# Kernel tuning notes

Measured on AMD Instinct MI355X. Metric: run time of the kernel, lower is better.

Reference implementation:

```python
import jax, jax.numpy as jnp
import numpy as np

NEG = -10000.0
EPS = 1e-5

B, N, H, DEPTH = 4096, 64, 128, 3
H2 = H // 2


def setup_inputs() -> dict:
    key = jax.random.key(0)
    k1, k2, k3 = jax.random.split(key, 3)
    hidden_states = jax.random.normal(k1, (B, N, H), dtype=jnp.float32)
    li_vector_num = jax.random.randint(k2, (B,), 0, N + 1, dtype=jnp.int32)
    Ws = jax.random.normal(k3, (DEPTH, H, H2), dtype=jnp.float32) * (1.0 / np.sqrt(H))
    bs = jnp.zeros((DEPTH, H2), dtype=jnp.float32)
    ln_w = jnp.ones((DEPTH, H2), dtype=jnp.float32)
    ln_b = jnp.zeros((DEPTH, H2), dtype=jnp.float32)
    return {"hidden_states": hidden_states, "li_vector_num": li_vector_num,
            "Ws": Ws, "bs": bs, "ln_w": ln_w, "ln_b": ln_b}


def _subgraph(hidden_states, Ws, bs, ln_w, ln_b, li_vector_num):
    b, n, h = hidden_states.shape
    # padding mask: -10000 for invalid vectors (i >= li_vector_num), per polyline
    pad = jnp.where(jnp.arange(n)[None, :] >= li_vector_num[:, None], NEG, 0.0)
    pad = pad.astype(hidden_states.dtype)[:, :, None]  # [B,N,1]
    hs = hidden_states
    for l in range(Ws.shape[0]):
        # MLP: linear -> layernorm -> relu
        x = jnp.einsum('bnh,hk->bnk', hs, Ws[l]) + bs[l]
        mu = jnp.mean(x, axis=-1, keepdims=True)
        var = jnp.mean((x - mu) ** 2, axis=-1, keepdims=True)
        x = ln_w[l] * (x - mu) * jax.lax.rsqrt(var + EPS) + ln_b[l]
        enc = jax.nn.relu(x)  # [B,N,H2]
        m = enc + pad  # masked encoded states
        # leave-one-out max over vector dim via top-2 trick (replaces O(N^2) loop)
        top2 = jax.lax.top_k(jnp.swapaxes(m, 1, 2), 2)[0]  # [B,H2,2]
        top1b = top2[..., 0][:, None, :]  # [B,1,H2]
        top2b = top2[..., 1][:, None, :]  # [B,1,H2]
        loo = jnp.where(m == top1b, top2b, top1b)  # max over i != j
        loo = jnp.maximum(loo, m + NEG)            # faithful: j itself at -10000
        loo = jnp.maximum(loo, 0.0)                # torch.max(max_hidden, zeros)
        hs = jnp.concatenate([enc, loo], axis=-1)  # [B,N,H]
    return jnp.max(hs, axis=1)  # [B,H]


def reference(hidden_states, li_vector_num, Ws, bs, ln_w, ln_b):
    return _subgraph(hidden_states, Ws, bs, ln_w, ln_b, li_vector_num)
```

## Files before the change

kernel.cpp:

```cpp
#include <hip/hip_runtime.h>
#include <hip/hip_bf16.h>

#define NEGV (-10000.0f)
#define EPSV (1e-5f)
#define NINF (-3.4e38f)

typedef __attribute__((ext_vector_type(8))) short short8;
typedef __attribute__((ext_vector_type(4))) float floatx4;

constexpr int Bsz = 4096, Nv = 64, Hd = 128, DEPTH = 3, H2 = 64;
constexpr int HSTR = 136;

struct alignas(8) BH4 { __hip_bfloat162 a, b; };

__device__ __forceinline__ unsigned short f2b(float f) {
    unsigned int u = __builtin_bit_cast(unsigned int, f);
    u += 0x7fffu + ((u >> 16) & 1u);
    return (unsigned short)(u >> 16);
}

__device__ __forceinline__ void t2ins(float& t1, float& t2, float v) {
    float lo = fminf(t1, v); t1 = fmaxf(t1, v); t2 = fmaxf(t2, lo);
}
__device__ __forceinline__ void t2merge(float& t1, float& t2, float o1, float o2) {
    float lo = fminf(t1, o1); t1 = fmaxf(t1, o1); t2 = fmaxf(fmaxf(t2, o2), lo);
}

__global__ void prep_w(const float* __restrict__ Ws, unsigned short* __restrict__ wt) {
    int idx = blockIdx.x * 256 + threadIdx.x;
    if (idx < DEPTH * 8192) {
        int l = idx >> 13, o = idx & 8191;
        int j = o & 7, q = (o >> 3) & 63, hi = (o >> 9) & 3, kt = o >> 11;
        int k = kt * 32 + hi * 8 + j;
        int srccol = (q & 15) * 4 + (q >> 4);
        wt[idx] = f2b(Ws[l * 8192 + k * 64 + srccol]);
    }
}

__global__ __launch_bounds__(256, 2)
void subgraph_kernel(const float* __restrict__ hidden, const int* __restrict__ lvn,
                     const unsigned short* __restrict__ wt,
                     const float* __restrict__ bsv, const float* __restrict__ lnw,
                     const float* __restrict__ lnb, float* __restrict__ out)
{
    __shared__ __hip_bfloat16 hsw[4][Nv][HSTR];

    const int t = threadIdx.x;
    const int lane = t & 63, wid = t >> 6;
    const int b = blockIdx.x * 4 + wid;
    const int lr = lane & 15, hi = lane >> 4;
    const int L = lvn[b];

    __hip_bfloat16 (*hs)[HSTR] = hsw[wid];

    float madd[4][4];
#pragma unroll
    for (int rt = 0; rt < 4; ++rt)
#pragma unroll
        for (int reg = 0; reg < 4; ++reg)
            madd[rt][reg] = ((rt * 16 + hi * 4 + reg) >= L) ? NEGV : 0.0f;

    const float4* ab = (const float4*)(hidden + (size_t)b * Nv * Hd);
    float encmax[4], loomax[4];

#pragma unroll
    for (int l = 0; l < DEPTH; ++l) {
        const short8* wfrag = (const short8*)(wt + l * 8192);

        floatx4 acc[4][4];
#pragma unroll
        for (int rt = 0; rt < 4; ++rt)
#pragma unroll
            for (int ct = 0; ct < 4; ++ct) { floatx4 z = {0.f,0.f,0.f,0.f}; acc[rt][ct] = z; }

#pragma unroll
        for (int kt = 0; kt < 4; ++kt) {
            short8 af[4];
            if (l == 0) {
#pragma unroll
                for (int rt = 0; rt < 4; ++rt) {
                    int fi = (rt * 16 + lr) * 32 + kt * 8 + hi * 2;
                    float4 f0 = ab[fi], f1 = ab[fi + 1];
                    union { short8 s; __hip_bfloat162 h[4]; } u;
                    u.h[0] = __float22bfloat162_rn(make_float2(f0.x, f0.y));
                    u.h[1] = __float22bfloat162_rn(make_float2(f0.z, f0.w));
                    u.h[2] = __float22bfloat162_rn(make_float2(f1.x, f1.y));
                    u.h[3] = __float22bfloat162_rn(make_float2(f1.z, f1.w));
                    af[rt] = u.s;
                }
            } else {
#pragma unroll
                for (int rt = 0; rt < 4; ++rt)
                    af[rt] = *(const short8*)&hs[rt * 16 + lr][kt * 32 + hi * 8];
            }
#pragma unroll
            for (int ct = 0; ct < 4; ++ct) {
                short8 bf = wfrag[(kt * 4 + hi) * 64 + ct * 16 + lr];
#pragma unroll
                for (int rt = 0; rt < 4; ++rt)
                    acc[rt][ct] = __builtin_amdgcn_mfma_f32_16x16x32_bf16(af[rt], bf, acc[rt][ct], 0, 0, 0);
            }
        }

        float4 bias = *(const float4*)(bsv + l * H2 + 4 * lr);
        float4 gw   = *(const float4*)(lnw + l * H2 + 4 * lr);
        float4 gb   = *(const float4*)(lnb + l * H2 + 4 * lr);
#pragma unroll
        for (int rt = 0; rt < 4; ++rt)
#pragma unroll
            for (int reg = 0; reg < 4; ++reg) {
                float x0 = acc[rt][0][reg] + bias.x;
                float x1 = acc[rt][1][reg] + bias.y;
                float x2 = acc[rt][2][reg] + bias.z;
                float x3 = acc[rt][3][reg] + bias.w;
                float s = x0 + x1 + x2 + x3;
                float q = x0 * x0 + x1 * x1 + x2 * x2 + x3 * x3;
#pragma unroll
                for (int m = 1; m < 16; m <<= 1) {
                    s += __shfl_xor(s, m, 64);
                    q += __shfl_xor(q, m, 64);
                }
                float mu  = s * (1.0f / 64.0f);
                float var = fmaxf(q * (1.0f / 64.0f) - mu * mu, 0.0f);
                float rstd = rsqrtf(var + EPSV);
                acc[rt][0][reg] = fmaxf(gw.x * (x0 - mu) * rstd + gb.x, 0.0f);
                acc[rt][1][reg] = fmaxf(gw.y * (x1 - mu) * rstd + gb.y, 0.0f);
                acc[rt][2][reg] = fmaxf(gw.z * (x2 - mu) * rstd + gb.z, 0.0f);
                acc[rt][3][reg] = fmaxf(gw.w * (x3 - mu) * rstd + gb.w, 0.0f);
            }

        float f1v[4], f2v[4];
#pragma unroll
        for (int ct = 0; ct < 4; ++ct) {
            float t1 = NINF, t2 = NINF;
#pragma unroll
            for (int rt = 0; rt < 4; ++rt)
#pragma unroll
                for (int reg = 0; reg < 4; ++reg)
                    t2ins(t1, t2, acc[rt][ct][reg] + madd[rt][reg]);
            t2merge(t1, t2, __shfl_xor(t1, 16, 64), __shfl_xor(t2, 16, 64));
            t2merge(t1, t2, __shfl_xor(t1, 32, 64), __shfl_xor(t2, 32, 64));
            f1v[ct] = t1; f2v[ct] = t2;
        }

        if (l < DEPTH - 1) {
#pragma unroll
            for (int rt = 0; rt < 4; ++rt)
#pragma unroll
                for (int reg = 0; reg < 4; ++reg) {
                    int row = rt * 16 + hi * 4 + reg;
                    float lo[4];
#pragma unroll
                    for (int ct = 0; ct < 4; ++ct) {
                        float mv = acc[rt][ct][reg] + madd[rt][reg];
                        float v = (mv == f1v[ct]) ? f2v[ct] : f1v[ct];
                        v = fmaxf(v, mv + NEGV);
                        lo[ct] = fmaxf(v, 0.0f);
                    }
                    BH4 we, wl_;
                    we.a  = __float22bfloat162_rn(make_float2(acc[rt][0][reg], acc[rt][1][reg]));
                    we.b  = __float22bfloat162_rn(make_float2(acc[rt][2][reg], acc[rt][3][reg]));
                    wl_.a = __float22bfloat162_rn(make_float2(lo[0], lo[1]));
                    wl_.b = __float22bfloat162_rn(make_float2(lo[2], lo[3]));
                    *(BH4*)&hs[row][4 * lr]      = we;
                    *(BH4*)&hs[row][64 + 4 * lr] = wl_;
                }
        } else {
#pragma unroll
            for (int ct = 0; ct < 4; ++ct) {
                float em = NINF, lm = NINF;
#pragma unroll
                for (int rt = 0; rt < 4; ++rt)
#pragma unroll
                    for (int reg = 0; reg < 4; ++reg) {
                        float e = acc[rt][ct][reg];
                        em = fmaxf(em, e);
                        float mv = e + madd[rt][reg];
                        float v = (mv == f1v[ct]) ? f2v[ct] : f1v[ct];
                        v = fmaxf(v, mv + NEGV);
                        lm = fmaxf(lm, fmaxf(v, 0.0f));
                    }
                em = fmaxf(em, __shfl_xor(em, 16, 64));
                em = fmaxf(em, __shfl_xor(em, 32, 64));
                lm = fmaxf(lm, __shfl_xor(lm, 16, 64));
                lm = fmaxf(lm, __shfl_xor(lm, 32, 64));
                encmax[ct] = em; loomax[ct] = lm;
            }
        }
    }

    if (hi == 0) {
        float4 e = make_float4(encmax[0], encmax[1], encmax[2], encmax[3]);
        float4 o = make_float4(loomax[0], loomax[1], loomax[2], loomax[3]);
        *(float4*)(out + (size_t)b * Hd + 4 * lr)      = e;
        *(float4*)(out + (size_t)b * Hd + 64 + 4 * lr) = o;
    }
}

extern "C" void kernel_launch(void* const* d_in, const int* in_sizes, int n_in,
                              void* d_out, int out_size, void* d_ws, size_t ws_size,
                              hipStream_t stream) {
    const float* hidden = (const float*)d_in[0];
    const int*   lvn    = (const int*)d_in[1];
    const float* Ws     = (const float*)d_in[2];
    const float* bs     = (const float*)d_in[3];
    const float* lnwp   = (const float*)d_in[4];
    const float* lnbp   = (const float*)d_in[5];
    unsigned short* wt  = (unsigned short*)d_ws;
    float* outp = (float*)d_out;

    prep_w<<<(DEPTH * 8192 + 255) / 256, 256, 0, stream>>>(Ws, wt);
    subgraph_kernel<<<Bsz / 4, 256, 0, stream>>>(hidden, lvn, wt, bs, lnwp, lnbp, outp);
}
```

Baseline: 68.26 us.

## Store only encoded states in LDS and recompute leave-one-out values on load

The kernel no longer stores the leave-one-out half in shared memory. It keeps only the bf16 encoded states plus a small per-column top1/top2 buffer, and rebuilds the leave-one-out operands while loading the MFMA A-fragments for the upper K tiles. This roughly halves LDS use per block so the launch bound can rise to 4 blocks per CU. The layernorm row reductions also switch from shuffles to DPP adds. In exchange, the leave-one-out selection math is repeated for every row tile of every K step, and the top-2 is now taken from bf16-rounded values, which slightly changes the equality test semantics.

```diff
diff --git a/kernel.cpp b/kernel.cpp
--- a/kernel.cpp
+++ b/kernel.cpp
@@ -9,7 +9,7 @@
 typedef __attribute__((ext_vector_type(4))) float floatx4;
 
 constexpr int Bsz = 4096, Nv = 64, Hd = 128, DEPTH = 3, H2 = 64;
-constexpr int HSTR = 136;
+constexpr int ESTR = 72;
 
 struct alignas(8) BH4 { __hip_bfloat162 a, b; };
 
@@ -17,6 +17,23 @@
     unsigned int u = __builtin_bit_cast(unsigned int, f);
     u += 0x7fffu + ((u >> 16) & 1u);
     return (unsigned short)(u >> 16);
+}
+__device__ __forceinline__ float b2f(short s) {
+    unsigned int u = ((unsigned int)(unsigned short)s) << 16;
+    return __builtin_bit_cast(float, u);
+}
+
+template <int CTRL>
+__device__ __forceinline__ float dpp_add(float v) {
+    int y = __builtin_amdgcn_update_dpp(0, __builtin_bit_cast(int, v), CTRL, 0xf, 0xf, true);
+    return v + __builtin_bit_cast(float, y);
+}
+__device__ __forceinline__ float sum16(float v) {
+    v = dpp_add<0xB1>(v);
+    v = dpp_add<0x4E>(v);
+    v = dpp_add<0x124>(v);
+    v = dpp_add<0x128>(v);
+    return v;
 }
 
 __device__ __forceinline__ void t2ins(float& t1, float& t2, float v) {
@@ -37,13 +54,14 @@
     }
 }
 
-__global__ __launch_bounds__(256, 2)
+__global__ __launch_bounds__(256, 4)
 void subgraph_kernel(const float* __restrict__ hidden, const int* __restrict__ lvn,
                      const unsigned short* __restrict__ wt,
                      const float* __restrict__ bsv, const float* __restrict__ lnw,
                      const float* __restrict__ lnb, float* __restrict__ out)
 {
-    __shared__ __hip_bfloat16 hsw[4][Nv][HSTR];
+    __shared__ __hip_bfloat16 encs[4][Nv][ESTR];
+    __shared__ float fbuf[4][128];
 
     const int t = threadIdx.x;
     const int lane = t & 63, wid = t >> 6;
@@ -51,14 +69,17 @@
     const int lr = lane & 15, hi = lane >> 4;
     const int L = lvn[b];
 
-    __hip_bfloat16 (*hs)[HSTR] = hsw[wid];
-
-    float madd[4][4];
-#pragma unroll
-    for (int rt = 0; rt < 4; ++rt)
+    __hip_bfloat16 (*enc_lds)[ESTR] = encs[wid];
+    float* fb = fbuf[wid];
+
+    float madd[4][4], maddA[4];
+#pragma unroll
+    for (int rt = 0; rt < 4; ++rt) {
 #pragma unroll
         for (int reg = 0; reg < 4; ++reg)
             madd[rt][reg] = ((rt * 16 + hi * 4 + reg) >= L) ? NEGV : 0.0f;
+        maddA[rt] = ((rt * 16 + lr) >= L) ? NEGV : 0.0f;
+    }
 
     const float4* ab = (const float4*)(hidden + (size_t)b * Nv * Hd);
     float encmax[4], loomax[4];
@@ -88,10 +109,35 @@
                     u.h[3] = __float22bfloat162_rn(make_float2(f1.z, f1.w));
                     af[rt] = u.s;
                 }
+            } else if (kt < 2) {
+#pragma unroll
+                for (int rt = 0; rt < 4; ++rt)
+                    af[rt] = *(const short8*)&enc_lds[rt * 16 + lr][kt * 32 + hi * 8];
             } else {
-#pragma unroll
-                for (int rt = 0; rt < 4; ++rt)
-                    af[rt] = *(const short8*)&hs[rt * 16 + lr][kt * 32 + hi * 8];
+                int fbase = (kt - 2) * 16 + 4 * hi;
+                float4 q0 = ((const float4*)fb)[fbase + 0];
+                float4 q1 = ((const float4*)fb)[fbase + 1];
+                float4 q2 = ((const float4*)fb)[fbase + 2];
+                float4 q3 = ((const float4*)fb)[fbase + 3];
+                float f1s[8] = {q0.x, q0.z, q1.x, q1.z, q2.x, q2.z, q3.x, q3.z};
+                float f2s[8] = {q0.y, q0.w, q1.y, q1.w, q2.y, q2.w, q3.y, q3.w};
+#pragma unroll
+                for (int rt = 0; rt < 4; ++rt) {
+                    short8 e = *(const short8*)&enc_lds[rt * 16 + lr][(kt - 2) * 32 + hi * 8];
+                    float lo[8];
+#pragma unroll
+                    for (int j = 0; j < 8; ++j) {
+                        float m = b2f(e[j]) + maddA[rt];
+                        float sel = (m == f1s[j]) ? f2s[j] : f1s[j];
+                        lo[j] = fmaxf(fmaxf(sel, m + NEGV), 0.0f);
+                    }
+                    union { short8 s; __hip_bfloat162 h[4]; } u;
+                    u.h[0] = __float22bfloat162_rn(make_float2(lo[0], lo[1]));
+                    u.h[1] = __float22bfloat162_rn(make_float2(lo[2], lo[3]));
+                    u.h[2] = __float22bfloat162_rn(make_float2(lo[4], lo[5]));
+                    u.h[3] = __float22bfloat162_rn(make_float2(lo[6], lo[7]));
+                    af[rt] = u.s;
+                }
             }
 #pragma unroll
             for (int ct = 0; ct < 4; ++ct) {
@@ -113,13 +159,8 @@
                 float x1 = acc[rt][1][reg] + bias.y;
                 float x2 = acc[rt][2][reg] + bias.z;
                 float x3 = acc[rt][3][reg] + bias.w;
-                float s = x0 + x1 + x2 + x3;
-                float q = x0 * x0 + x1 * x1 + x2 * x2 + x3 * x3;
-#pragma unroll
-                for (int m = 1; m < 16; m <<= 1) {
-                    s += __shfl_xor(s, m, 64);
-                    q += __shfl_xor(q, m, 64);
-                }
+                float s = sum16((x0 + x1) + (x2 + x3));
+                float q = sum16((x0 * x0 + x1 * x1) + (x2 * x2 + x3 * x3));
                 float mu  = s * (1.0f / 64.0f);
                 float var = fmaxf(q * (1.0f / 64.0f) - mu * mu, 0.0f);
                 float rstd = rsqrtf(var + EPSV);
@@ -129,43 +170,47 @@
                 acc[rt][3][reg] = fmaxf(gw.w * (x3 - mu) * rstd + gb.w, 0.0f);
             }
 
-        float f1v[4], f2v[4];
-#pragma unroll
-        for (int ct = 0; ct < 4; ++ct) {
-            float t1 = NINF, t2 = NINF;
-#pragma unroll
-            for (int rt = 0; rt < 4; ++rt)
-#pragma unroll
-                for (int reg = 0; reg < 4; ++reg)
-                    t2ins(t1, t2, acc[rt][ct][reg] + madd[rt][reg]);
-            t2merge(t1, t2, __shfl_xor(t1, 16, 64), __shfl_xor(t2, 16, 64));
-            t2merge(t1, t2, __shfl_xor(t1, 32, 64), __shfl_xor(t2, 32, 64));
-            f1v[ct] = t1; f2v[ct] = t2;
-        }
-
         if (l < DEPTH - 1) {
+            float t1[4] = {NINF, NINF, NINF, NINF}, t2[4] = {NINF, NINF, NINF, NINF};
 #pragma unroll
             for (int rt = 0; rt < 4; ++rt)
 #pragma unroll
                 for (int reg = 0; reg < 4; ++reg) {
                     int row = rt * 16 + hi * 4 + reg;
-                    float lo[4];
-#pragma unroll
-                    for (int ct = 0; ct < 4; ++ct) {
-                        float mv = acc[rt][ct][reg] + madd[rt][reg];
-                        float v = (mv == f1v[ct]) ? f2v[ct] : f1v[ct];
-                        v = fmaxf(v, mv + NEGV);
-                        lo[ct] = fmaxf(v, 0.0f);
-                    }
-                    BH4 we, wl_;
-                    we.a  = __float22bfloat162_rn(make_float2(acc[rt][0][reg], acc[rt][1][reg]));
-                    we.b  = __float22bfloat162_rn(make_float2(acc[rt][2][reg], acc[rt][3][reg]));
-                    wl_.a = __float22bfloat162_rn(make_float2(lo[0], lo[1]));
-                    wl_.b = __float22bfloat162_rn(make_float2(lo[2], lo[3]));
-                    *(BH4*)&hs[row][4 * lr]      = we;
-                    *(BH4*)&hs[row][64 + 4 * lr] = wl_;
+                    BH4 we;
+                    we.a = __float22bfloat162_rn(make_float2(acc[rt][0][reg], acc[rt][1][reg]));
+                    we.b = __float22bfloat162_rn(make_float2(acc[rt][2][reg], acc[rt][3][reg]));
+                    *(BH4*)&enc_lds[row][4 * lr] = we;
+                    t2ins(t1[0], t2[0], __bfloat162float(we.a.x) + madd[rt][reg]);
+                    t2ins(t1[1], t2[1], __bfloat162float(we.a.y) + madd[rt][reg]);
+                    t2ins(t1[2], t2[2], __bfloat162float(we.b.x) + madd[rt][reg]);
+                    t2ins(t1[3], t2[3], __bfloat162float(we.b.y) + madd[rt][reg]);
                 }
+#pragma unroll
+            for (int ct = 0; ct < 4; ++ct) {
+                t2merge(t1[ct], t2[ct], __shfl_xor(t1[ct], 16, 64), __shfl_xor(t2[ct], 16, 64));
+                t2merge(t1[ct], t2[ct], __shfl_xor(t1[ct], 32, 64), __shfl_xor(t2[ct], 32, 64));
+            }
+            if (hi == 0) {
+                float4 w0 = make_float4(t1[0], t2[0], t1[1], t2[1]);
+                float4 w1 = make_float4(t1[2], t2[2], t1[3], t2[3]);
+                ((float4*)fb)[2 * lr]     = w0;
+                ((float4*)fb)[2 * lr + 1] = w1;
+            }
         } else {
+            float f1v[4], f2v[4];
+#pragma unroll
+            for (int ct = 0; ct < 4; ++ct) {
+                float t1 = NINF, t2 = NINF;
+#pragma unroll
+                for (int rt = 0; rt < 4; ++rt)
+#pragma unroll
+                    for (int reg = 0; reg < 4; ++reg)
+                        t2ins(t1, t2, acc[rt][ct][reg] + madd[rt][reg]);
+                t2merge(t1, t2, __shfl_xor(t1, 16, 64), __shfl_xor(t2, 16, 64));
+                t2merge(t1, t2, __shfl_xor(t1, 32, 64), __shfl_xor(t2, 32, 64));
+                f1v[ct] = t1; f2v[ct] = t2;
+            }
 #pragma unroll
             for (int ct = 0; ct < 4; ++ct) {
                 float em = NINF, lm = NINF;
```

Measured after the change: 109.8 us. +60.9%, slower.
